# Kernel tuning notes

Hardware: AMD Instinct MI355X
Metric: run time of the kernel (lower is better)

Reference implementation:

```python
import jax, jax.numpy as jnp
import numpy as np

BN_EPS = 1e-5


def setup_inputs() -> dict:
    key = jax.random.key(0)
    ks = jax.random.split(key, 8)
    b, c, h, w, d = 16, 256, 128, 128, 64
    x = jax.random.normal(ks[0], (b, c, h, w), dtype=jnp.float32)
    conv1_w = jax.random.normal(ks[1], (c, c), dtype=jnp.float32) * np.sqrt(2.0 / c)
    conv1_b = jax.random.normal(ks[2], (c,), dtype=jnp.float32) * 0.02
    mk_w = jax.random.normal(ks[3], (d, c), dtype=jnp.float32) * np.sqrt(2.0 / d)
    mv_w = jnp.transpose(mk_w)  # original ties mv.weight = mk.weight.permute(1,0,2)
    conv2_w = jax.random.normal(ks[4], (c, c), dtype=jnp.float32) * np.sqrt(2.0 / c)
    bn_gamma = jnp.ones((c,), dtype=jnp.float32)
    bn_beta = jnp.zeros((c,), dtype=jnp.float32)
    bn_mean = jax.random.normal(ks[5], (c,), dtype=jnp.float32) * 0.1
    bn_var = jax.random.uniform(ks[6], (c,), dtype=jnp.float32, minval=0.5, maxval=1.5)
    return {"x": x, "conv1_w": conv1_w, "conv1_b": conv1_b, "mk_w": mk_w,
            "mv_w": mv_w, "conv2_w": conv2_w, "bn_gamma": bn_gamma,
            "bn_beta": bn_beta, "bn_mean": bn_mean, "bn_var": bn_var}


def reference(x, conv1_w, conv1_b, mk_w, mv_w, conv2_w, bn_gamma, bn_beta, bn_mean, bn_var):
    b, c, h, w = x.shape
    n = h * w
    identity = x
    # conv1: 1x1 conv with bias -> [b, c, n]
    y = jnp.einsum('oc,bchw->bohw', conv1_w, x) + conv1_b[None, :, None, None]
    y = y.reshape(b, c, n)
    # external attention: mk projection [b, d, n]
    attn = jnp.einsum('dc,bcn->bdn', mk_w, y)
    attn = jax.nn.softmax(attn, axis=-1)              # softmax over spatial N
    attn = attn / (1e-9 + attn.sum(axis=1, keepdims=True))  # column-normalize over d
    # mv projection back to channels [b, c, n]
    z = jnp.einsum('cd,bdn->bcn', mv_w, attn)
    z = z.reshape(b, c, h, w)
    # conv2 (1x1, no bias) + BatchNorm (inference) + residual + relu
    z = jnp.einsum('oc,bchw->bohw', conv2_w, z)
    inv = bn_gamma / jnp.sqrt(bn_var + BN_EPS)
    z = z * inv[None, :, None, None] + (bn_beta - bn_mean * inv)[None, :, None, None]
    return jax.nn.relu(z + identity)
```

## Files before the change

### kernel.cpp

```cpp
#include <hip/hip_runtime.h>

#define HW 16384
#define C  256
#define D  64
#define NB 16

typedef unsigned short u16;
typedef __attribute__((ext_vector_type(4))) float  f32x4;
typedef __attribute__((ext_vector_type(4))) short  s16x4;
typedef __attribute__((ext_vector_type(8))) short  s16x8;

__device__ __forceinline__ float fast_exp(float v) {
    return exp2f(v * 1.44269504088896340736f);
}
__device__ __forceinline__ float bf2f(u16 u) {
    return __uint_as_float(((unsigned int)u) << 16);
}
__device__ __forceinline__ u16 f2bf(float f) {
    unsigned int u = __float_as_uint(f);
    unsigned int r = (u + 0x7fffu + ((u >> 16) & 1u)) >> 16;
    return (u16)r;
}

#define MFMA16(a, b, c) __builtin_amdgcn_mfma_f32_16x16x32_bf16((a), (b), (c), 0, 0, 0)

__global__ void precompute_kernel(const float* __restrict__ conv1_w,
                                  const float* __restrict__ conv1_b,
                                  const float* __restrict__ mk_w,
                                  const float* __restrict__ mv_w,
                                  const float* __restrict__ conv2_w,
                                  const float* __restrict__ gamma,
                                  const float* __restrict__ beta,
                                  const float* __restrict__ mean,
                                  const float* __restrict__ var,
                                  short* __restrict__ Ath,
                                  short* __restrict__ Atl,
                                  float* __restrict__ amk,
                                  short* __restrict__ Bmb,
                                  float* __restrict__ shift)
{
    int gid = blockIdx.x * blockDim.x + threadIdx.x;
    if (gid < C * D) {
        int d = gid >> 8, cp = gid & 255;
        float s = 0.f;
        for (int c = 0; c < C; ++c) s += mk_w[d * C + c] * conv1_w[c * C + cp];
        u16 h = f2bf(s);
        Ath[gid] = (short)h;
        Atl[gid] = (short)f2bf(s - bf2f(h));
    } else if (gid < 2 * C * D) {
        int g = gid - C * D;
        int o = g >> 6, d = g & 63;
        float inv = gamma[o] * rsqrtf(var[o] + 1e-5f);
        float s = 0.f;
        for (int c = 0; c < C; ++c) s += conv2_w[o * C + c] * mv_w[c * D + d];
        Bmb[g] = (short)f2bf(s * inv);
    } else if (gid < 2 * C * D + D) {
        int d = gid - 2 * C * D;
        float s = 0.f;
        for (int c = 0; c < C; ++c) s += mk_w[d * C + c] * conv1_b[c];
        amk[d] = s;
    } else if (gid < 2 * C * D + D + C) {
        int o = gid - (2 * C * D + D);
        float inv = gamma[o] * rsqrtf(var[o] + 1e-5f);
        shift[o] = beta[o] - mean[o] * inv;
    }
}

#define NT1 64
#define XR  (C + 8)
__global__ __launch_bounds__(256, 3) void logits_kernel(const float* __restrict__ x,
                                                        const short* __restrict__ Ath,
                                                        const short* __restrict__ Atl,
                                                        const float* __restrict__ amk,
                                                        u16* __restrict__ logits)
{
    __shared__ short xs[NT1 * XR];
    const int t = threadIdx.x;
    const int b = blockIdx.y;
    const int n0 = blockIdx.x * NT1;
    const int lane = t & 63, w = t >> 6;
    const int col = lane & 15, g = lane >> 4;

    const float* xb = x + (size_t)b * C * HW + n0;
    #pragma unroll
    for (int i = 0; i < 4; ++i) {
        int cell = i * 256 + t;
        int nq = cell & 15, cq = cell >> 4;
        int c0 = cq * 4, nn = nq * 4;
        const float* gp = xb + (size_t)c0 * HW + nn;
        f32x4 r0 = *(const f32x4*)(gp);
        f32x4 r1 = *(const f32x4*)(gp + HW);
        f32x4 r2 = *(const f32x4*)(gp + 2 * HW);
        f32x4 r3 = *(const f32x4*)(gp + 3 * HW);
        #pragma unroll
        for (int j = 0; j < 4; ++j) {
            s16x4 hi = { (short)f2bf(r0[j]), (short)f2bf(r1[j]),
                         (short)f2bf(r2[j]), (short)f2bf(r3[j]) };
            *(s16x4*)&xs[(nn + j) * XR + c0] = hi;
        }
    }
    __syncthreads();

    s16x8 Ah[8], Al[8];
    {
        const short* ah = Ath + (size_t)(w * 16 + col) * C + 8 * g;
        const short* al = Atl + (size_t)(w * 16 + col) * C + 8 * g;
        #pragma unroll
        for (int ks = 0; ks < 8; ++ks) {
            Ah[ks] = *(const s16x8*)(ah + ks * 32);
            Al[ks] = *(const s16x8*)(al + ks * 32);
        }
    }

    f32x4 zz = {0.f, 0.f, 0.f, 0.f};
    f32x4 acc[4] = { zz, zz, zz, zz };
    #pragma unroll
    for (int ks = 0; ks < 8; ++ks) {
        #pragma unroll
        for (int nt = 0; nt < 4; ++nt) {
            s16x8 xf = *(const s16x8*)&xs[(nt * 16 + col) * XR + ks * 32 + 8 * g];
            acc[nt] = MFMA16(xf, Ah[ks], acc[nt]);
            acc[nt] = MFMA16(xf, Al[ks], acc[nt]);
        }
    }

    const float am = amk[w * 16 + col];
    u16* lb = logits + (size_t)b * D * HW + (size_t)(w * 16 + col) * HW + n0;
    #pragma unroll
    for (int nt = 0; nt < 4; ++nt) {
        s16x4 st4;
        #pragma unroll
        for (int r = 0; r < 4; ++r) st4[r] = (short)f2bf(acc[nt][r] + am);
        *(s16x4*)(lb + nt * 16 + 4 * g) = st4;
    }
}

__global__ __launch_bounds__(256) void stats_kernel(const u16* __restrict__ logits,
                                                    float* __restrict__ stats)
{
    const int row = blockIdx.x;
    const s16x4* lr = (const s16x4*)(logits + (size_t)row * HW);
    const int t = threadIdx.x;
    const int lane = t & 63, wid = t >> 6;

    float v[64];
    float m = -3.402823466e+38f;
    #pragma unroll
    for (int i = 0; i < 16; ++i) {
        s16x4 q = lr[t + i * 256];
        #pragma unroll
        for (int k = 0; k < 4; ++k) {
            float f = bf2f((u16)q[k]);
            v[i * 4 + k] = f;
            m = fmaxf(m, f);
        }
    }
    #pragma unroll
    for (int off = 1; off < 64; off <<= 1) m = fmaxf(m, __shfl_xor(m, off));

    __shared__ float redm[4];
    if (lane == 0) redm[wid] = m;
    __syncthreads();
    const float bm = fmaxf(fmaxf(redm[0], redm[1]), fmaxf(redm[2], redm[3]));

    float s = 0.f;
    #pragma unroll
    for (int i = 0; i < 64; ++i) s += fast_exp(v[i] - bm);
    #pragma unroll
    for (int off = 1; off < 64; off <<= 1) s += __shfl_xor(s, off);

    __shared__ float reds[4];
    if (lane == 0) reds[wid] = s;
    __syncthreads();
    if (t == 0) {
        float S = reds[0] + reds[1] + reds[2] + reds[3];
        stats[2 * row]     = bm;
        stats[2 * row + 1] = 1.0f / S;
    }
}

#define NT3 64
__global__ __launch_bounds__(256, 3) void out_kernel(const float* __restrict__ x,
                                                     const u16* __restrict__ logits,
                                                     const float* __restrict__ stats,
                                                     const short* __restrict__ Bmb,
                                                     const float* __restrict__ shift,
                                                     float* __restrict__ out)
{
    __shared__ short ps[NT3 * 72];
    __shared__ float csum[4][NT3];
    __shared__ float rr[NT3];

    const int t = threadIdx.x;
    const int b = blockIdx.y;
    const int n0 = blockIdx.x * NT3;

    {
        const int nl = t & 63, dq = t >> 6;
        const u16* lg = logits + (size_t)b * D * HW + (size_t)(dq * 16) * HW + n0 + nl;
        const float* st = stats + 2 * (b * D + dq * 16);
        float cs = 0.f;
        #pragma unroll
        for (int j4 = 0; j4 < 4; ++j4) {
            s16x4 pk;
            #pragma unroll
            for (int jj = 0; jj < 4; ++jj) {
                int j = j4 * 4 + jj;
                float pv = fast_exp(bf2f(lg[(size_t)j * HW]) - st[2 * j]) * st[2 * j + 1];
                cs += pv;
                pk[jj] = (short)f2bf(pv);
            }
            *(s16x4*)&ps[nl * 72 + dq * 16 + j4 * 4] = pk;
        }
        csum[dq][nl] = cs;
    }
    __syncthreads();
    if (t < NT3)
        rr[t] = 1.0f / (csum[0][t] + csum[1][t] + csum[2][t] + csum[3][t] + 1e-9f);
    __syncthreads();

    const int lane = t & 63, col = lane & 15, g = lane >> 4;
    const int w = t >> 6;

    s16x8 Bf[4][2];
    #pragma unroll
    for (int ot = 0; ot < 4; ++ot) {
        const short* bp = Bmb + (size_t)(w * 64 + ot * 16 + col) * D + 8 * g;
        Bf[ot][0] = *(const s16x8*)(bp);
        Bf[ot][1] = *(const s16x8*)(bp + 32);
    }

    f32x4 zz = {0.f, 0.f, 0.f, 0.f};
    f32x4 acc[4][4];
    #pragma unroll
    for (int ot = 0; ot < 4; ++ot)
        #pragma unroll
        for (int nt = 0; nt < 4; ++nt) acc[ot][nt] = zz;

    #pragma unroll
    for (int nt = 0; nt < 4; ++nt) {
        const short* pr = &ps[(nt * 16 + col) * 72 + 8 * g];
        s16x8 p0 = *(const s16x8*)(pr);
        s16x8 p1 = *(const s16x8*)(pr + 32);
        #pragma unroll
        for (int ot = 0; ot < 4; ++ot) {
            acc[ot][nt] = MFMA16(p0, Bf[ot][0], acc[ot][nt]);
            acc[ot][nt] = MFMA16(p1, Bf[ot][1], acc[ot][nt]);
        }
    }

    float sh[4];
    #pragma unroll
    for (int ot = 0; ot < 4; ++ot) sh[ot] = shift[w * 64 + ot * 16 + col];

    const float* xb = x + (size_t)b * C * HW + n0;
    float* ob = out + (size_t)b * C * HW + n0;
    #pragma unroll
    for (int nt = 0; nt < 4; ++nt) {
        f32x4 rv = *(const f32x4*)&rr[nt * 16 + 4 * g];
        #pragma unroll
        for (int ot = 0; ot < 4; ++ot) {
            const size_t off = (size_t)(w * 64 + ot * 16 + col) * HW + nt * 16 + 4 * g;
            f32x4 xv = *(const f32x4*)(xb + off);
            f32x4 vv;
            #pragma unroll
            for (int r = 0; r < 4; ++r)
                vv[r] = fmaxf(acc[ot][nt][r] * rv[r] + sh[ot] + xv[r], 0.f);
            *(f32x4*)(ob + off) = vv;
        }
    }
}

extern "C" void kernel_launch(void* const* d_in, const int* in_sizes, int n_in,
                              void* d_out, int out_size, void* d_ws, size_t ws_size,
                              hipStream_t stream)
{
    const float* x       = (const float*)d_in[0];
    const float* conv1_w = (const float*)d_in[1];
    const float* conv1_b = (const float*)d_in[2];
    const float* mk_w    = (const float*)d_in[3];
    const float* mv_w    = (const float*)d_in[4];
    const float* conv2_w = (const float*)d_in[5];
    const float* gamma   = (const float*)d_in[6];
    const float* beta    = (const float*)d_in[7];
    const float* mean    = (const float*)d_in[8];
    const float* var     = (const float*)d_in[9];
    float* out = (float*)d_out;

    float* amk   = (float*)d_ws;
    float* shift = amk + D;
    float* stats = shift + C;
    short* Ath   = (short*)(stats + 2 * NB * D);
    short* Atl   = Ath + C * D;
    short* Bmb   = Atl + C * D;
    u16* logits  = (u16*)(Bmb + C * D);

    const int pre_work = 2 * C * D + D + C;
    precompute_kernel<<<(pre_work + 255) / 256, 256, 0, stream>>>(
        conv1_w, conv1_b, mk_w, mv_w, conv2_w, gamma, beta, mean, var,
        Ath, Atl, amk, Bmb, shift);

    logits_kernel<<<dim3(HW / NT1, NB), 256, 0, stream>>>(x, Ath, Atl, amk, logits);

    stats_kernel<<<NB * D, 256, 0, stream>>>(logits, stats);

    out_kernel<<<dim3(HW / NT3, NB), 256, 0, stream>>>(x, logits, stats, Bmb, shift, out);
}
```

Measured before the change: 588.1 us.

## Fuse softmax exponent and row sums into logits kernel, drop stats pass

The logits kernel now computes exp(logit - 16) directly, stores the bf16 exponentials, and accumulates per-row sums with atomics into a buffer zeroed by the precompute kernel. This removes the separate max/sum stats kernel, its extra pass over the logits buffer, and the exp in the output kernel. The fixed offset replaces the true row max, so it can overflow or underflow if logits leave roughly ±88 around 16. The output kernel also walks blocks in reverse order to reuse recently written data in cache, and uses nontemporal stores for the output.

```diff
diff --git a/kernel.cpp b/kernel.cpp
--- a/kernel.cpp
+++ b/kernel.cpp
@@ -1,20 +1,24 @@
 #include <hip/hip_runtime.h>
+#include <hip/hip_bf16.h>
 
 #define HW 16384
 #define C  256
 #define D  64
 #define NB 16
+#define M0 16.0f
 
 typedef unsigned short u16;
 typedef __attribute__((ext_vector_type(4))) float  f32x4;
 typedef __attribute__((ext_vector_type(4))) short  s16x4;
 typedef __attribute__((ext_vector_type(8))) short  s16x8;
 
-__device__ __forceinline__ float fast_exp(float v) {
-    return exp2f(v * 1.44269504088896340736f);
-}
 __device__ __forceinline__ float bf2f(u16 u) {
     return __uint_as_float(((unsigned int)u) << 16);
+}
+__device__ __forceinline__ short f2bfs(float f) {
+    union { __hip_bfloat16 h; short s; } u;
+    u.h = __float2bfloat16(f);
+    return u.s;
 }
 __device__ __forceinline__ u16 f2bf(float f) {
     unsigned int u = __float_as_uint(f);
@@ -37,7 +41,8 @@
                                   short* __restrict__ Atl,
                                   float* __restrict__ amk,
                                   short* __restrict__ Bmb,
-                                  float* __restrict__ shift)
+                                  float* __restrict__ shift,
+                                  float* __restrict__ esum)
 {
     int gid = blockIdx.x * blockDim.x + threadIdx.x;
     if (gid < C * D) {
@@ -63,16 +68,19 @@
         int o = gid - (2 * C * D + D);
         float inv = gamma[o] * rsqrtf(var[o] + 1e-5f);
         shift[o] = beta[o] - mean[o] * inv;
+    } else if (gid < 2 * C * D + D + C + NB * D) {
+        esum[gid - (2 * C * D + D + C)] = 0.f;
     }
 }
 
 #define NT1 64
 #define XR  (C + 8)
-__global__ __launch_bounds__(256, 3) void logits_kernel(const float* __restrict__ x,
-                                                        const short* __restrict__ Ath,
-                                                        const short* __restrict__ Atl,
-                                                        const float* __restrict__ amk,
-                                                        u16* __restrict__ logits)
+__global__ __launch_bounds__(256, 3) void pexp_kernel(const float* __restrict__ x,
+                                                      const short* __restrict__ Ath,
+                                                      const short* __restrict__ Atl,
+                                                      const float* __restrict__ amk,
+                                                      u16* __restrict__ pexp,
+                                                      float* __restrict__ esum)
 {
     __shared__ short xs[NT1 * XR];
     const int t = threadIdx.x;
@@ -94,8 +102,7 @@
         f32x4 r3 = *(const f32x4*)(gp + 3 * HW);
         #pragma unroll
         for (int j = 0; j < 4; ++j) {
-            s16x4 hi = { (short)f2bf(r0[j]), (short)f2bf(r1[j]),
-                         (short)f2bf(r2[j]), (short)f2bf(r3[j]) };
+            s16x4 hi = { f2bfs(r0[j]), f2bfs(r1[j]), f2bfs(r2[j]), f2bfs(r3[j]) };
             *(s16x4*)&xs[(nn + j) * XR + c0] = hi;
         }
     }
@@ -125,64 +132,28 @@
     }
 
     const float am = amk[w * 16 + col];
-    u16* lb = logits + (size_t)b * D * HW + (size_t)(w * 16 + col) * HW + n0;
+    u16* pb = pexp + (size_t)b * D * HW + (size_t)(w * 16 + col) * HW + n0;
+    float rs = 0.f;
     #pragma unroll
     for (int nt = 0; nt < 4; ++nt) {
         s16x4 st4;
         #pragma unroll
-        for (int r = 0; r < 4; ++r) st4[r] = (short)f2bf(acc[nt][r] + am);
-        *(s16x4*)(lb + nt * 16 + 4 * g) = st4;
-    }
-}
-
-__global__ __launch_bounds__(256) void stats_kernel(const u16* __restrict__ logits,
-                                                    float* __restrict__ stats)
-{
-    const int row = blockIdx.x;
-    const s16x4* lr = (const s16x4*)(logits + (size_t)row * HW);
-    const int t = threadIdx.x;
-    const int lane = t & 63, wid = t >> 6;
-
-    float v[64];
-    float m = -3.402823466e+38f;
-    #pragma unroll
-    for (int i = 0; i < 16; ++i) {
-        s16x4 q = lr[t + i * 256];
-        #pragma unroll
-        for (int k = 0; k < 4; ++k) {
-            float f = bf2f((u16)q[k]);
-            v[i * 4 + k] = f;
-            m = fmaxf(m, f);
-        }
-    }
-    #pragma unroll
-    for (int off = 1; off < 64; off <<= 1) m = fmaxf(m, __shfl_xor(m, off));
-
-    __shared__ float redm[4];
-    if (lane == 0) redm[wid] = m;
-    __syncthreads();
-    const float bm = fmaxf(fmaxf(redm[0], redm[1]), fmaxf(redm[2], redm[3]));
-
-    float s = 0.f;
-    #pragma unroll
-    for (int i = 0; i < 64; ++i) s += fast_exp(v[i] - bm);
-    #pragma unroll
-    for (int off = 1; off < 64; off <<= 1) s += __shfl_xor(s, off);
-
-    __shared__ float reds[4];
-    if (lane == 0) reds[wid] = s;
-    __syncthreads();
-    if (t == 0) {
-        float S = reds[0] + reds[1] + reds[2] + reds[3];
-        stats[2 * row]     = bm;
-        stats[2 * row + 1] = 1.0f / S;
-    }
+        for (int r = 0; r < 4; ++r) {
+            float e = exp2f((acc[nt][r] + am - M0) * 1.44269504088896340736f);
+            rs += e;
+            st4[r] = f2bfs(e);
+        }
+        *(s16x4*)(pb + nt * 16 + 4 * g) = st4;
+    }
+    rs += __shfl_xor(rs, 16);
+    rs += __shfl_xor(rs, 32);
+    if (lane < 16) atomicAdd(esum + b * D + w * 16 + lane, rs);
 }
 
 #define NT3 64
 __global__ __launch_bounds__(256, 3) void out_kernel(const float* __restrict__ x,
-                                                     const u16* __restrict__ logits,
-                                                     const float* __restrict__ stats,
+                                                     const u16* __restrict__ pexp,
+                                                     const float* __restrict__ esum,
                                                      const short* __restrict__ Bmb,
                                                      const float* __restrict__ shift,
                                                      float* __restrict__ out)
@@ -192,13 +163,13 @@
     __shared__ float rr[NT3];
 
     const int t = threadIdx.x;
-    const int b = blockIdx.y;
-    const int n0 = blockIdx.x * NT3;
+    const int b  = (NB - 1) - blockIdx.y;
+    const int n0 = ((int)gridDim.x - 1 - blockIdx.x) * NT3;
 
     {
         const int nl = t & 63, dq = t >> 6;
-        const u16* lg = logits + (size_t)b * D * HW + (size_t)(dq * 16) * HW + n0 + nl;
-        const float* st = stats + 2 * (b * D + dq * 16);
+        const u16* lg = pexp + (size_t)b * D * HW + (size_t)(dq * 16) * HW + n0 + nl;
+        const float* es = esum + b * D + dq * 16;
         float cs = 0.f;
         #pragma unroll
         for (int j4 = 0; j4 < 4; ++j4) {
@@ -206,9 +177,10 @@
             #pragma unroll
             for (int jj = 0; jj < 4; ++jj) {
                 int j = j4 * 4 + jj;
-                float pv = fast_exp(bf2f(lg[(size_t)j * HW]) - st[2 * j]) * st[2 * j + 1];
+                float iv = __fdividef(1.0f, es[j]);
+                float pv = bf2f(lg[(size_t)j * HW]) * iv;
                 cs += pv;
-                pk[jj] = (short)f2bf(pv);
+                pk[jj] = f2bfs(pv);
             }
             *(s16x4*)&ps[nl * 72 + dq * 16 + j4 * 4] = pk;
         }
@@ -216,7 +188,7 @@
     }
     __syncthreads();
     if (t < NT3)
-        rr[t] = 1.0f / (csum[0][t] + csum[1][t] + csum[2][t] + csum[3][t] + 1e-9f);
+        rr[t] = __fdividef(1.0f, csum[0][t] + csum[1][t] + csum[2][t] + csum[3][t] + 1e-9f);
     __syncthreads();
 
     const int lane = t & 63, col = lane & 15, g = lane >> 4;
@@ -266,7 +238,7 @@
             #pragma unroll
             for (int r = 0; r < 4; ++r)
                 vv[r] = fmaxf(acc[ot][nt][r] * rv[r] + sh[ot] + xv[r], 0.f);
-            *(f32x4*)(ob + off) = vv;
+            __builtin_nontemporal_store(vv, (f32x4*)(ob + off));
         }
     }
 }
@@ -289,20 +261,18 @@
 
     float* amk   = (float*)d_ws;
     float* shift = amk + D;
-    float* stats = shift + C;
-    short* Ath   = (short*)(stats + 2 * NB * D);
+    float* esum  = shift + C;
+    short* Ath   = (short*)(esum + NB * D);
     short* Atl   = Ath + C * D;
     short* Bmb   = Atl + C * D;
-    u16* logits  = (u16*)(Bmb + C * D);
-
-    const int pre_work = 2 * C * D + D + C;
+    u16* pexp    = (u16*)(Bmb + C * D);
+
+    const int pre_work = 2 * C * D + D + C + NB * D;
     precompute_kernel<<<(pre_work + 255) / 256, 256, 0, stream>>>(
         conv1_w, conv1_b, mk_w, mv_w, conv2_w, gamma, beta, mean, var,
-        Ath, Atl, amk, Bmb, shift);
-
-    logits_kernel<<<dim3(HW / NT1, NB), 256, 0, stream>>>(x, Ath, Atl, amk, logits);
-
-    stats_kernel<<<NB * D, 256, 0, stream>>>(logits, stats);
-
-    out_kernel<<<dim3(HW / NT3, NB), 256, 0, stream>>>(x, logits, stats, Bmb, shift, out);
-}
+        Ath, Atl, amk, Bmb, shift, esum);
+
+    pexp_kernel<<<dim3(HW / NT1, NB), 256, 0, stream>>>(x, Ath, Atl, amk, pexp, esum);
+
+    out_kernel<<<dim3(HW / NT3, NB), 256, 0, stream>>>(x, pexp, esum, Bmb, shift, out);
+}
```

After: 544.2 us. 7.5% less time.
